# Optimization experiments

Hardware: AMD Instinct MI355X
Metric: run time of the kernel (lower is better)

## Reference

```python
import jax, jax.numpy as jnp
import numpy as np

B, N, D, H, DEG = 2, 20000, 256, 8, 8
E = N * DEG
EPS = 1e-3  # keras LayerNormalization default epsilon


def layer_norm(x, gamma, beta):
    mu = jnp.mean(x, axis=-1, keepdims=True)
    var = jnp.mean(jnp.square(x - mu), axis=-1, keepdims=True)
    return (x - mu) * jax.lax.rsqrt(var + EPS) * gamma + beta


def setup_inputs() -> dict:
    key = jax.random.key(0)
    ks = jax.random.split(key, 8)
    x = jax.random.normal(ks[0], (B, N, D), dtype=jnp.float32)
    # edge list sorted by source node; every node has DEG out-edges so
    # segment_sum covers all N segments (matches tf.math.segment_sum semantics)
    src = jnp.repeat(jnp.arange(N, dtype=jnp.int64), DEG)
    dst = jax.random.randint(ks[1], (E,), 0, N, dtype=jnp.int64)
    edges = jnp.stack([src, dst], axis=1)  # [E, 2]
    scale = 0.05
    wq = jax.random.normal(ks[2], (D, D), dtype=jnp.float32) * scale
    wk = jax.random.normal(ks[3], (D, D), dtype=jnp.float32) * scale
    wv = jax.random.normal(ks[4], (D, D), dtype=jnp.float32) * scale
    wo = jax.random.normal(ks[5], (D, D), dtype=jnp.float32) * scale
    zeros = jnp.zeros((D,), dtype=jnp.float32)
    ones = jnp.ones((D,), dtype=jnp.float32)
    return {
        "x": x, "edges": edges,
        "wq": wq, "bq": zeros, "wk": wk, "bk": zeros,
        "wv": wv, "bv": zeros, "wo": wo, "bo": zeros,
        "gamma1": ones, "beta1": zeros, "gamma2": ones, "beta2": zeros,
    }


def reference(x, edges, wq, bq, wk, bk, wv, bv, wo, bo, gamma1, beta1, gamma2, beta2):
    b, n, d = x.shape
    h, dh = H, D // H
    xn = layer_norm(x, gamma1, beta1)                      # [B,N,D]
    # QKV projections, split heads, move node axis to front: [N,B,H,dh]
    def proj(w, bias):
        y = (xn @ w + bias).reshape(b, n, h, dh)
        return jnp.transpose(y, (1, 0, 2, 3))
    q, k, v = proj(wq, bq), proj(wk, bk), proj(wv, bv)
    src, dst = edges[:, 0], edges[:, 1]
    q_part = q[src]                                         # [E,B,H,dh]
    k_part = k[dst]
    v_part = v[dst]
    logits = jnp.sum(q_part * k_part, axis=-1, keepdims=True) / jnp.sqrt(
        jnp.asarray(dh, dtype=x.dtype))                     # [E,B,H,1]
    w = jnp.exp(logits)                                     # unnormalized softmax (as in source)
    num = jax.ops.segment_sum(v_part * w, src, num_segments=n)  # [N,B,H,dh]
    den = jax.ops.segment_sum(w, src, num_segments=n)           # [N,B,H,1]
    attn = num / den
    attn = jnp.transpose(attn, (1, 0, 2, 3)).reshape(b, n, d)   # [B,N,D]
    concat = xn + attn                                      # residual uses normed input (source reassigns `inputs`)
    out = layer_norm(concat, gamma2, beta2)
    out = jax.nn.relu(out @ wo + bo)
    return out + concat
```

## Files before the change

### kernel.cpp

```cpp
#include <hip/hip_runtime.h>


typedef __bf16 bf16x8 __attribute__((ext_vector_type(8)));
typedef float  f32x4  __attribute__((ext_vector_type(4)));

__device__ __forceinline__ float bf2f(unsigned short u) {
    union { unsigned int i; float f; } v; v.i = ((unsigned int)u) << 16; return v.f;
}
__device__ __forceinline__ unsigned short f2bf(float f) {
    union { float f; unsigned int i; } v; v.f = f;
    unsigned int x = v.i;
    unsigned int r = (x + 0x7FFFu + ((x >> 16) & 1u)) >> 16;
    return (unsigned short)r;
}

#define NNODE 20000
#define ROWS  40000
#define DMODEL 256

__global__ __launch_bounds__(256) void prep_ln1_kernel(
    const float* __restrict__ wq, const float* __restrict__ wk,
    const float* __restrict__ wv, const float* __restrict__ wo,
    const float* __restrict__ bq, const float* __restrict__ bk,
    const float* __restrict__ bv, const float* __restrict__ bo,
    const float* __restrict__ x,
    const float* __restrict__ g1, const float* __restrict__ b1,
    unsigned short* __restrict__ Wqkvt,
    unsigned short* __restrict__ Wot,
    float* __restrict__ biasq,
    float* __restrict__ biaso,
    unsigned short* __restrict__ xn)
{
    if (blockIdx.x < 1024) {
        int idx = blockIdx.x * 256 + threadIdx.x;
        if (idx < 768 * 256) {
            int n = idx >> 8, k = idx & 255;
            int sel = n >> 8, nl = n & 255;
            const float* w = (sel == 0) ? wq : (sel == 1) ? wk : wv;
            Wqkvt[idx] = f2bf(w[k * 256 + nl]);
        } else {
            int idx2 = idx - 768 * 256;
            int n = idx2 >> 8, k = idx2 & 255;
            Wot[idx2] = f2bf(wo[k * 256 + n]);
        }
        if (idx < 768) {
            const float* bb = (idx < 256) ? bq : (idx < 512) ? bk : bv;
            biasq[idx] = bb[idx & 255];
        }
        if (idx >= 768 && idx < 1024) biaso[idx - 768] = bo[idx - 768];
        return;
    }
    int wave = threadIdx.x >> 6, lane = threadIdx.x & 63;
    int sub = lane >> 5, hl = lane & 31;
    int m = (blockIdx.x - 1024) * 8 + wave * 2 + sub;
    const float* xp = x + (size_t)m * DMODEL + hl * 8;
    float4 x0 = *(const float4*)xp;
    float4 x1 = *(const float4*)(xp + 4);
    float f[8] = {x0.x, x0.y, x0.z, x0.w, x1.x, x1.y, x1.z, x1.w};
    float s = 0.f, ss = 0.f;
    #pragma unroll
    for (int t = 0; t < 8; ++t) { s += f[t]; ss += f[t]*f[t]; }
    #pragma unroll
    for (int mk = 1; mk < 32; mk <<= 1) { s += __shfl_xor(s, mk); ss += __shfl_xor(ss, mk); }
    float mu  = s * (1.f/256.f);
    float var = ss * (1.f/256.f) - mu*mu;
    float rs  = rsqrtf(var + 1e-3f);
    float4 g0 = *(const float4*)(g1 + hl * 8);
    float4 g1v = *(const float4*)(g1 + hl * 8 + 4);
    float4 b0 = *(const float4*)(b1 + hl * 8);
    float4 b1v = *(const float4*)(b1 + hl * 8 + 4);
    float gg[8] = {g0.x, g0.y, g0.z, g0.w, g1v.x, g1v.y, g1v.z, g1v.w};
    float bb[8] = {b0.x, b0.y, b0.z, b0.w, b1v.x, b1v.y, b1v.z, b1v.w};
    unsigned short o[8];
    #pragma unroll
    for (int t = 0; t < 8; ++t) o[t] = f2bf((f[t] - mu) * rs * gg[t] + bb[t]);
    *(int4*)(xn + (size_t)m * DMODEL + hl * 8) = *(const int4*)o;
}

#define LDS_W 72
#define MFMA_BF16(d, a, b) d = __builtin_amdgcn_mfma_f32_16x16x32_bf16(a, b, d, 0, 0, 0)

template<bool EPI>
__global__ __launch_bounds__(256, 2) void gemm_kernel(
    const unsigned short* __restrict__ A,
    const unsigned short* __restrict__ Bt,
    const float* __restrict__ bias,
    void* __restrict__ C,
    const unsigned short* __restrict__ resid,
    int M, int Ncols)
{
    __shared__ unsigned short As[128 * LDS_W];
    __shared__ unsigned short Bs[128 * LDS_W];
    int tid  = threadIdx.x;
    int wave = tid >> 6, lane = tid & 63;
    int quad = lane >> 4, l16 = lane & 15;
    int m0 = blockIdx.x * 128, n0 = blockIdx.y * 128;
    int wm = (wave >> 1) * 64, wn = (wave & 1) * 64;

    int srow = tid >> 1;
    int sseg = (tid & 1) * 32;
    int arow = m0 + srow; if (arow >= M) arow = M - 1;
    const unsigned short* ArowP = A  + (size_t)arow * 256 + sseg;
    const unsigned short* BrowP = Bt + (size_t)(n0 + srow) * 256 + sseg;
    unsigned short* AsP = &As[srow * LDS_W + sseg];
    unsigned short* BsP = &Bs[srow * LDS_W + sseg];

    f32x4 acc00 = {}, acc01 = {}, acc02 = {}, acc03 = {};
    f32x4 acc10 = {}, acc11 = {}, acc12 = {}, acc13 = {};
    f32x4 acc20 = {}, acc21 = {}, acc22 = {}, acc23 = {};
    f32x4 acc30 = {}, acc31 = {}, acc32 = {}, acc33 = {};

    for (int kt = 0; kt < 4; ++kt) {
        const unsigned short* ap = ArowP + kt * 64;
        const unsigned short* bp = BrowP + kt * 64;
        int4 va0 = *(const int4*)(ap);
        int4 va1 = *(const int4*)(ap + 8);
        int4 va2 = *(const int4*)(ap + 16);
        int4 va3 = *(const int4*)(ap + 24);
        int4 vb0 = *(const int4*)(bp);
        int4 vb1 = *(const int4*)(bp + 8);
        int4 vb2 = *(const int4*)(bp + 16);
        int4 vb3 = *(const int4*)(bp + 24);
        __syncthreads();
        *(int4*)(AsP)      = va0;
        *(int4*)(AsP + 8)  = va1;
        *(int4*)(AsP + 16) = va2;
        *(int4*)(AsP + 24) = va3;
        *(int4*)(BsP)      = vb0;
        *(int4*)(BsP + 8)  = vb1;
        *(int4*)(BsP + 16) = vb2;
        *(int4*)(BsP + 24) = vb3;
        __syncthreads();
        #pragma unroll
        for (int ks = 0; ks < 64; ks += 32) {
            bf16x8 a0 = *(const bf16x8*)&As[(wm +  0 + l16) * LDS_W + ks + quad * 8];
            bf16x8 a1 = *(const bf16x8*)&As[(wm + 16 + l16) * LDS_W + ks + quad * 8];
            bf16x8 a2 = *(const bf16x8*)&As[(wm + 32 + l16) * LDS_W + ks + quad * 8];
            bf16x8 a3 = *(const bf16x8*)&As[(wm + 48 + l16) * LDS_W + ks + quad * 8];
            bf16x8 b0 = *(const bf16x8*)&Bs[(wn +  0 + l16) * LDS_W + ks + quad * 8];
            bf16x8 b1 = *(const bf16x8*)&Bs[(wn + 16 + l16) * LDS_W + ks + quad * 8];
            bf16x8 b2 = *(const bf16x8*)&Bs[(wn + 32 + l16) * LDS_W + ks + quad * 8];
            bf16x8 b3 = *(const bf16x8*)&Bs[(wn + 48 + l16) * LDS_W + ks + quad * 8];
            MFMA_BF16(acc00, a0, b0); MFMA_BF16(acc01, a0, b1);
            MFMA_BF16(acc02, a0, b2); MFMA_BF16(acc03, a0, b3);
            MFMA_BF16(acc10, a1, b0); MFMA_BF16(acc11, a1, b1);
            MFMA_BF16(acc12, a1, b2); MFMA_BF16(acc13, a1, b3);
            MFMA_BF16(acc20, a2, b0); MFMA_BF16(acc21, a2, b1);
            MFMA_BF16(acc22, a2, b2); MFMA_BF16(acc23, a2, b3);
            MFMA_BF16(acc30, a3, b0); MFMA_BF16(acc31, a3, b1);
            MFMA_BF16(acc32, a3, b2); MFMA_BF16(acc33, a3, b3);
        }
    }

#define EPI_STORE(accv, R, CC) do {                                          \
        int col = n0 + wn + (CC) * 16 + l16;                                 \
        float bb = bias[col];                                                \
        int rowb = m0 + wm + (R) * 16 + quad * 4;                            \
        _Pragma("unroll")                                                    \
        for (int rr = 0; rr < 4; ++rr) {                                     \
            int row = rowb + rr;                                             \
            if (row < M) {                                                   \
                float v = (accv)[rr] + bb;                                   \
                if (EPI) {                                                   \
                    v = fmaxf(v, 0.f);                                       \
                    v += bf2f(resid[(size_t)row * 256 + col]);               \
                    ((float*)C)[(size_t)row * Ncols + col] = v;              \
                } else {                                                     \
                    ((unsigned short*)C)[(size_t)row * Ncols + col] = f2bf(v);\
                }                                                            \
            }                                                                \
        }                                                                    \
    } while (0)

    EPI_STORE(acc00, 0, 0); EPI_STORE(acc01, 0, 1); EPI_STORE(acc02, 0, 2); EPI_STORE(acc03, 0, 3);
    EPI_STORE(acc10, 1, 0); EPI_STORE(acc11, 1, 1); EPI_STORE(acc12, 1, 2); EPI_STORE(acc13, 1, 3);
    EPI_STORE(acc20, 2, 0); EPI_STORE(acc21, 2, 1); EPI_STORE(acc22, 2, 2); EPI_STORE(acc23, 2, 3);
    EPI_STORE(acc30, 3, 0); EPI_STORE(acc31, 3, 1); EPI_STORE(acc32, 3, 2); EPI_STORE(acc33, 3, 3);
#undef EPI_STORE
}

__global__ __launch_bounds__(256) void attn_kernel(
    const unsigned short* __restrict__ qkv,
    const int* __restrict__ edges,
    const unsigned short* __restrict__ xn,
    const float* __restrict__ g2, const float* __restrict__ b2,
    unsigned short* __restrict__ concat,
    unsigned short* __restrict__ h2)
{
    int wave = threadIdx.x >> 6, lane = threadIdx.x & 63;
    int i = blockIdx.x * 4 + wave;
    int b = lane >> 5, hl = lane & 31;
    size_t m = (size_t)b * NNODE + i;

    int4 qi = *(const int4*)(qkv + m * 768 + hl * 8);
    const unsigned short* qs = (const unsigned short*)&qi;
    float qf[8];
    #pragma unroll
    for (int t = 0; t < 8; ++t) qf[t] = bf2f(qs[t]);

    int jv = 0;
    if (lane < 8) jv = edges[2 * (i * 8 + lane) + 1];

#define KVLOAD(E)                                                                  \
    int j##E = __shfl(jv, E);                                                      \
    const unsigned short* kp##E = qkv + ((size_t)b * NNODE + j##E) * 768 + 256 + hl * 8; \
    int4 KI##E = *(const int4*)(kp##E);                                            \
    int4 VI##E = *(const int4*)(kp##E + 256);
    KVLOAD(0) KVLOAD(1) KVLOAD(2) KVLOAD(3)
    KVLOAD(4) KVLOAD(5) KVLOAD(6) KVLOAD(7)
#undef KVLOAD

    float acc[8] = {};
    float den = 0.f;
    const float scale = 0.17677669529663687f;
#define EDGE(E) do {                                                         \
        const unsigned short* ks = (const unsigned short*)&KI##E;            \
        const unsigned short* vs = (const unsigned short*)&VI##E;            \
        float dot = 0.f;                                                     \
        _Pragma("unroll")                                                    \
        for (int t = 0; t < 8; ++t) dot += qf[t] * bf2f(ks[t]);              \
        dot += __shfl_xor(dot, 1);                                           \
        dot += __shfl_xor(dot, 2);               \
        float w = __expf(dot * scale);                                       \
        _Pragma("unroll")                                                    \
        for (int t = 0; t < 8; ++t) acc[t] += w * bf2f(vs[t]);               \
        den += w;                                                            \
    } while (0)
    EDGE(0); EDGE(1); EDGE(2); EDGE(3);
    EDGE(4); EDGE(5); EDGE(6); EDGE(7);
#undef EDGE
    float inv = 1.f / den;

    int4 xi = *(const int4*)(xn + m * DMODEL + hl * 8);
    const unsigned short* xs = (const unsigned short*)&xi;
    float c[8], s = 0.f, ss = 0.f;
    #pragma unroll
    for (int t = 0; t < 8; ++t) { c[t] = bf2f(xs[t]) + acc[t] * inv; s += c[t]; ss += c[t]*c[t]; }
    #pragma unroll
    for (int mk = 1; mk < 32; mk <<= 1) { s += __shfl_xor(s, mk); ss += __shfl_xor(ss, mk); }
    float mu  = s * (1.f/256.f);
    float var = ss * (1.f/256.f) - mu*mu;
    float rs  = rsqrtf(var + 1e-3f);

    float4 ga = *(const float4*)(g2 + hl * 8);
    float4 gb = *(const float4*)(g2 + hl * 8 + 4);
    float4 ba = *(const float4*)(b2 + hl * 8);
    float4 bb = *(const float4*)(b2 + hl * 8 + 4);
    float gg[8] = {ga.x, ga.y, ga.z, ga.w, gb.x, gb.y, gb.z, gb.w};
    float bv[8] = {ba.x, ba.y, ba.z, ba.w, bb.x, bb.y, bb.z, bb.w};
    unsigned short oc[8], oh[8];
    #pragma unroll
    for (int t = 0; t < 8; ++t) {
        oc[t] = f2bf(c[t]);
        oh[t] = f2bf((c[t] - mu) * rs * gg[t] + bv[t]);
    }
    *(int4*)(concat + m * DMODEL + hl * 8) = *(const int4*)oc;
    *(int4*)(h2     + m * DMODEL + hl * 8) = *(const int4*)oh;
}

extern "C" void kernel_launch(void* const* d_in, const int* in_sizes, int n_in,
                              void* d_out, int out_size, void* d_ws, size_t ws_size,
                              hipStream_t stream)
{
    const float* x   = (const float*)d_in[0];
    const int* edges = (const int*)d_in[1];
    const float* wq = (const float*)d_in[2];
    const float* bq = (const float*)d_in[3];
    const float* wk = (const float*)d_in[4];
    const float* bk = (const float*)d_in[5];
    const float* wv = (const float*)d_in[6];
    const float* bv = (const float*)d_in[7];
    const float* wo = (const float*)d_in[8];
    const float* bo = (const float*)d_in[9];
    const float* g1 = (const float*)d_in[10];
    const float* b1 = (const float*)d_in[11];
    const float* g2 = (const float*)d_in[12];
    const float* b2 = (const float*)d_in[13];

    char* ws = (char*)d_ws;
    unsigned short* Wqkvt = (unsigned short*)(ws);
    unsigned short* Wot   = (unsigned short*)(ws + 393216);
    float* biasq          = (float*)(ws + 393216 + 131072);
    float* biaso          = (float*)(ws + 393216 + 131072 + 3072);
    size_t off = 393216 + 131072 + 4096;
    unsigned short* xn     = (unsigned short*)(ws + off); off += (size_t)ROWS * DMODEL * 2;
    unsigned short* qkv    = (unsigned short*)(ws + off); off += (size_t)ROWS * 768 * 2;
    unsigned short* concat = (unsigned short*)(ws + off); off += (size_t)ROWS * DMODEL * 2;
    unsigned short* h2     = (unsigned short*)(ws + off); off += (size_t)ROWS * DMODEL * 2;

    prep_ln1_kernel<<<1024 + ROWS / 8, 256, 0, stream>>>(
        wq, wk, wv, wo, bq, bk, bv, bo, x, g1, b1, Wqkvt, Wot, biasq, biaso, xn);
    gemm_kernel<false><<<dim3(313, 6), 256, 0, stream>>>(xn, Wqkvt, biasq, qkv, nullptr, ROWS, 768);
    attn_kernel<<<NNODE / 4, 256, 0, stream>>>(qkv, edges, xn, g2, b2, concat, h2);
    gemm_kernel<true><<<dim3(313, 2), 256, 0, stream>>>(h2, Wot, biaso, d_out, concat, ROWS, 256);
}
```

Measured before the change: 236.8 us.

## Restructure GEMMs to stage full-K A rows in LDS and stream weights from global

```diff
diff --git a/kernel.cpp b/kernel.cpp
--- a/kernel.cpp
+++ b/kernel.cpp
@@ -77,106 +77,93 @@
     *(int4*)(xn + (size_t)m * DMODEL + hl * 8) = *(const int4*)o;
 }
 
-#define LDS_W 72
+#define AS_W 264
 #define MFMA_BF16(d, a, b) d = __builtin_amdgcn_mfma_f32_16x16x32_bf16(a, b, d, 0, 0, 0)
 
-template<bool EPI>
-__global__ __launch_bounds__(256, 2) void gemm_kernel(
+template<bool EPI, int NCHUNK>
+__global__ __launch_bounds__(256, 2) void gemm2_kernel(
     const unsigned short* __restrict__ A,
     const unsigned short* __restrict__ Bt,
     const float* __restrict__ bias,
     void* __restrict__ C,
     const unsigned short* __restrict__ resid,
-    int M, int Ncols)
-{
-    __shared__ unsigned short As[128 * LDS_W];
-    __shared__ unsigned short Bs[128 * LDS_W];
+    int Ncols)
+{
+    __shared__ unsigned short As[64 * AS_W];
     int tid  = threadIdx.x;
     int wave = tid >> 6, lane = tid & 63;
     int quad = lane >> 4, l16 = lane & 15;
-    int m0 = blockIdx.x * 128, n0 = blockIdx.y * 128;
-    int wm = (wave >> 1) * 64, wn = (wave & 1) * 64;
-
-    int srow = tid >> 1;
-    int sseg = (tid & 1) * 32;
-    int arow = m0 + srow; if (arow >= M) arow = M - 1;
-    const unsigned short* ArowP = A  + (size_t)arow * 256 + sseg;
-    const unsigned short* BrowP = Bt + (size_t)(n0 + srow) * 256 + sseg;
-    unsigned short* AsP = &As[srow * LDS_W + sseg];
-    unsigned short* BsP = &Bs[srow * LDS_W + sseg];
-
-    f32x4 acc00 = {}, acc01 = {}, acc02 = {}, acc03 = {};
-    f32x4 acc10 = {}, acc11 = {}, acc12 = {}, acc13 = {};
-    f32x4 acc20 = {}, acc21 = {}, acc22 = {}, acc23 = {};
-    f32x4 acc30 = {}, acc31 = {}, acc32 = {}, acc33 = {};
-
-    for (int kt = 0; kt < 4; ++kt) {
-        const unsigned short* ap = ArowP + kt * 64;
-        const unsigned short* bp = BrowP + kt * 64;
-        int4 va0 = *(const int4*)(ap);
-        int4 va1 = *(const int4*)(ap + 8);
-        int4 va2 = *(const int4*)(ap + 16);
-        int4 va3 = *(const int4*)(ap + 24);
-        int4 vb0 = *(const int4*)(bp);
-        int4 vb1 = *(const int4*)(bp + 8);
-        int4 vb2 = *(const int4*)(bp + 16);
-        int4 vb3 = *(const int4*)(bp + 24);
-        __syncthreads();
-        *(int4*)(AsP)      = va0;
-        *(int4*)(AsP + 8)  = va1;
-        *(int4*)(AsP + 16) = va2;
-        *(int4*)(AsP + 24) = va3;
-        *(int4*)(BsP)      = vb0;
-        *(int4*)(BsP + 8)  = vb1;
-        *(int4*)(BsP + 16) = vb2;
-        *(int4*)(BsP + 24) = vb3;
-        __syncthreads();
+    int m0 = blockIdx.x * 64;
+
+    {
+        int r = tid >> 2, c = (tid & 3) * 64;
+        const unsigned short* src = A + (size_t)(m0 + r) * 256 + c;
+        unsigned short* dst = &As[r * AS_W + c];
+        int4 t0 = *(const int4*)(src);
+        int4 t1 = *(const int4*)(src + 8);
+        int4 t2 = *(const int4*)(src + 16);
+        int4 t3 = *(const int4*)(src + 24);
+        int4 t4 = *(const int4*)(src + 32);
+        int4 t5 = *(const int4*)(src + 40);
+        int4 t6 = *(const int4*)(src + 48);
+        int4 t7 = *(const int4*)(src + 56);
+        *(int4*)(dst)      = t0;
+        *(int4*)(dst + 8)  = t1;
+        *(int4*)(dst + 16) = t2;
+        *(int4*)(dst + 24) = t3;
+        *(int4*)(dst + 32) = t4;
+        *(int4*)(dst + 40) = t5;
+        *(int4*)(dst + 48) = t6;
+        *(int4*)(dst + 56) = t7;
+    }
+    __syncthreads();
+
+    #pragma unroll
+    for (int s = 0; s < NCHUNK; ++s) {
+        int col0 = wave * 32 + s * 128;
+        const unsigned short* Bp = Bt + (size_t)(col0 + l16) * 256 + quad * 8;
+
+        f32x4 c0a = {}, c0b = {}, c1a = {}, c1b = {};
+        f32x4 c2a = {}, c2b = {}, c3a = {}, c3b = {};
+
         #pragma unroll
-        for (int ks = 0; ks < 64; ks += 32) {
-            bf16x8 a0 = *(const bf16x8*)&As[(wm +  0 + l16) * LDS_W + ks + quad * 8];
-            bf16x8 a1 = *(const bf16x8*)&As[(wm + 16 + l16) * LDS_W + ks + quad * 8];
-            bf16x8 a2 = *(const bf16x8*)&As[(wm + 32 + l16) * LDS_W + ks + quad * 8];
-            bf16x8 a3 = *(const bf16x8*)&As[(wm + 48 + l16) * LDS_W + ks + quad * 8];
-            bf16x8 b0 = *(const bf16x8*)&Bs[(wn +  0 + l16) * LDS_W + ks + quad * 8];
-            bf16x8 b1 = *(const bf16x8*)&Bs[(wn + 16 + l16) * LDS_W + ks + quad * 8];
-            bf16x8 b2 = *(const bf16x8*)&Bs[(wn + 32 + l16) * LDS_W + ks + quad * 8];
-            bf16x8 b3 = *(const bf16x8*)&Bs[(wn + 48 + l16) * LDS_W + ks + quad * 8];
-            MFMA_BF16(acc00, a0, b0); MFMA_BF16(acc01, a0, b1);
-            MFMA_BF16(acc02, a0, b2); MFMA_BF16(acc03, a0, b3);
-            MFMA_BF16(acc10, a1, b0); MFMA_BF16(acc11, a1, b1);
-            MFMA_BF16(acc12, a1, b2); MFMA_BF16(acc13, a1, b3);
-            MFMA_BF16(acc20, a2, b0); MFMA_BF16(acc21, a2, b1);
-            MFMA_BF16(acc22, a2, b2); MFMA_BF16(acc23, a2, b3);
-            MFMA_BF16(acc30, a3, b0); MFMA_BF16(acc31, a3, b1);
-            MFMA_BF16(acc32, a3, b2); MFMA_BF16(acc33, a3, b3);
+        for (int kt = 0; kt < 8; ++kt) {
+            bf16x8 a0 = *(const bf16x8*)&As[( 0 + l16) * AS_W + kt * 32 + quad * 8];
+            bf16x8 a1 = *(const bf16x8*)&As[(16 + l16) * AS_W + kt * 32 + quad * 8];
+            bf16x8 a2 = *(const bf16x8*)&As[(32 + l16) * AS_W + kt * 32 + quad * 8];
+            bf16x8 a3 = *(const bf16x8*)&As[(48 + l16) * AS_W + kt * 32 + quad * 8];
+            bf16x8 b0 = *(const bf16x8*)(Bp + kt * 32);
+            bf16x8 b1 = *(const bf16x8*)(Bp + 16 * 256 + kt * 32);
+            MFMA_BF16(c0a, a0, b0); MFMA_BF16(c0b, a0, b1);
+            MFMA_BF16(c1a, a1, b0); MFMA_BF16(c1b, a1, b1);
+            MFMA_BF16(c2a, a2, b0); MFMA_BF16(c2b, a2, b1);
+            MFMA_BF16(c3a, a3, b0); MFMA_BF16(c3b, a3, b1);
         }
-    }
-
-#define EPI_STORE(accv, R, CC) do {                                          \
-        int col = n0 + wn + (CC) * 16 + l16;                                 \
+
+#define EPI_ST(accv, RF, CF) do {                                            \
+        int col = col0 + (CF) * 16 + l16;                                    \
         float bb = bias[col];                                                \
-        int rowb = m0 + wm + (R) * 16 + quad * 4;                            \
+        int rowb = m0 + (RF) * 16 + quad * 4;                                \
         _Pragma("unroll")                                                    \
         for (int rr = 0; rr < 4; ++rr) {                                     \
             int row = rowb + rr;                                             \
-            if (row < M) {                                                   \
-                float v = (accv)[rr] + bb;                                   \
-                if (EPI) {                                                   \
-                    v = fmaxf(v, 0.f);                                       \
-                    v += bf2f(resid[(size_t)row * 256 + col]);               \
-                    ((float*)C)[(size_t)row * Ncols + col] = v;              \
-                } else {                                                     \
-                    ((unsigned short*)C)[(size_t)row * Ncols + col] = f2bf(v);\
-                }                                                            \
+            float v = (accv)[rr] + bb;                                       \
+            if (EPI) {                                                       \
+                v = fmaxf(v, 0.f);                                           \
+                v += bf2f(resid[(size_t)row * 256 + col]);                   \
+                ((float*)C)[(size_t)row * Ncols + col] = v;                  \
+            } else {                                                         \
+                ((unsigned short*)C)[(size_t)row * Ncols + col] = f2bf(v);   \
             }                                                                \
         }                                                                    \
     } while (0)
 
-    EPI_STORE(acc00, 0, 0); EPI_STORE(acc01, 0, 1); EPI_STORE(acc02, 0, 2); EPI_STORE(acc03, 0, 3);
-    EPI_STORE(acc10, 1, 0); EPI_STORE(acc11, 1, 1); EPI_STORE(acc12, 1, 2); EPI_STORE(acc13, 1, 3);
-    EPI_STORE(acc20, 2, 0); EPI_STORE(acc21, 2, 1); EPI_STORE(acc22, 2, 2); EPI_STORE(acc23, 2, 3);
-    EPI_STORE(acc30, 3, 0); EPI_STORE(acc31, 3, 1); EPI_STORE(acc32, 3, 2); EPI_STORE(acc33, 3, 3);
-#undef EPI_STORE
+        EPI_ST(c0a, 0, 0); EPI_ST(c0b, 0, 1);
+        EPI_ST(c1a, 1, 0); EPI_ST(c1b, 1, 1);
+        EPI_ST(c2a, 2, 0); EPI_ST(c2b, 2, 1);
+        EPI_ST(c3a, 3, 0); EPI_ST(c3b, 3, 1);
+#undef EPI_ST
+    }
 }
 
 __global__ __launch_bounds__(256) void attn_kernel(
@@ -290,7 +277,7 @@
 
     prep_ln1_kernel<<<1024 + ROWS / 8, 256, 0, stream>>>(
         wq, wk, wv, wo, bq, bk, bv, bo, x, g1, b1, Wqkvt, Wot, biasq, biaso, xn);
-    gemm_kernel<false><<<dim3(313, 6), 256, 0, stream>>>(xn, Wqkvt, biasq, qkv, nullptr, ROWS, 768);
+    gemm2_kernel<false, 6><<<625, 256, 0, stream>>>(xn, Wqkvt, biasq, qkv, nullptr, 768);
     attn_kernel<<<NNODE / 4, 256, 0, stream>>>(qkv, edges, xn, g2, b2, concat, h2);
-    gemm_kernel<true><<<dim3(313, 2), 256, 0, stream>>>(h2, Wot, biaso, d_out, concat, ROWS, 256);
-}
+    gemm2_kernel<true, 2><<<625, 256, 0, stream>>>(h2, Wot, biaso, d_out, concat, 256);
+}
```

After: 255.5 us. +7.9%, slower.
